# Kernel optimization log

Hardware: AMD Instinct MI355X
Metric: run time of the kernel (lower is better)

## Reference

```python
import jax, jax.numpy as jnp
import numpy as np

UP = 2
CUTOFF = 1.0 / UP  # factor = 1


def make_recon_rect(N, cutoff):
    """Reconstruction low-pass rect for rfft2, shape [N, N//2+1]."""
    lo = int(N * cutoff // 2)
    hi = int(N - lo)
    r = np.ones(N, dtype=np.float32)
    r[lo + 1:hi] = 0.0
    if N % 4 == 0:
        r[lo] = 0.5
        r[hi] = 0.5
    rect2d = r[:, None] * r[None, :]          # [N, N]
    return jnp.asarray(rect2d[:, :N // 2 + 1])  # keep rfft half-spectrum


def setup_inputs() -> dict:
    key = jax.random.key(0)
    x = jax.random.normal(key, (16, 64, 128, 128), dtype=jnp.float32)
    return {"x": x}


def reference(x):
    B, C, H, W = x.shape
    Hu, Wu = H * UP, W * UP
    # zero-insertion upsample: sample at (i*UP, j*UP), zeros elsewhere
    z = jnp.zeros((B, C, Hu, Wu), dtype=x.dtype).at[:, :, ::UP, ::UP].set(x)
    rect = make_recon_rect(Wu, CUTOFF)         # [Wu, Wu//2+1]
    xf = jnp.fft.rfft2(z) * rect               # low-pass in frequency domain
    out = jnp.fft.irfft2(xf) * (UP ** 2)       # gain correction
    return out
```

## Files before the change

### kernel.cpp

```cpp
#include <hip/hip_runtime.h>


typedef __bf16 bf16x8 __attribute__((ext_vector_type(8)));
typedef float  f32x4  __attribute__((ext_vector_type(4)));

#define W2 136
#define PI_F 3.14159265358979323846f

__device__ __forceinline__ unsigned short f2bf(float x) {
    unsigned int b = __float_as_uint(x);
    return (unsigned short)((b + 0x7FFFu + ((b >> 16) & 1u)) >> 16);
}

__device__ __forceinline__ float gfun(int j) {
    int d = 2 * (j & 127) + 1;
    float th = PI_F * (float)d * (1.0f / 256.0f);
    float s  = ((d & 3) == 1) ? 1.0f : -1.0f;
    return s * cosf(th) / (128.0f * sinf(th));
}

__global__ __launch_bounds__(512)
void init_ghtab(unsigned short* __restrict__ ghtab)
{
    const int t    = threadIdx.x;
    const int lane = t & 63;
    const int l15  = lane & 15;
    const int l4   = lane >> 4;
    const int dd   = t >> 6;
    const int base = l15 - 8 * l4 + 16 * dd;
    unsigned short u[8];
    #pragma unroll
    for (int e = 0; e < 8; ++e) u[e] = f2bf(gfun(base - e));
    *(ushort4*)&ghtab[t * 8]     = make_ushort4(u[0], u[1], u[2], u[3]);
    *(ushort4*)&ghtab[t * 8 + 4] = make_ushort4(u[4], u[5], u[6], u[7]);
}

__global__ __launch_bounds__(512, 4)
void upsample_fused(const float* __restrict__ xin, float* __restrict__ out,
                    const unsigned short* __restrict__ ghtab)
{
    __shared__ __align__(16) unsigned short Et[128 * W2];

    const int tid  = threadIdx.x;
    const int lane = tid & 63;
    const int w    = tid >> 6;
    const int l15  = lane & 15;
    const int l4   = lane >> 4;

    const long long img = blockIdx.x >> 1;
    const int cb        = blockIdx.x & 1;
    const float* __restrict__ xim = xin + img * (128LL * 128LL);
    float*       __restrict__ oim = out + img * (256LL * 256LL);

    const int r = 16 * w + l15;
    const float* __restrict__ xrow = xim + r * 128;

    float4 xlo[4], xhi[4];
    #pragma unroll
    for (int t = 0; t < 4; ++t) {
        xlo[t] = *(const float4*)&xrow[32 * t + 8 * l4];
        xhi[t] = *(const float4*)&xrow[32 * t + 8 * l4 + 4];
    }

    bf16x8 ghc[8];
    #pragma unroll
    for (int v = 0; v < 8; ++v) {
        const int dd = (v + 4 * cb) & 7;
        ghc[v] = *(const bf16x8*)&ghtab[(dd * 64 + lane) * 8];
    }

    bf16x8 xa[4];
    #pragma unroll
    for (int t = 0; t < 4; ++t) {
        union { bf16x8 v; unsigned short u[8]; } H;
        H.u[0] = f2bf(xlo[t].x); H.u[1] = f2bf(xlo[t].y);
        H.u[2] = f2bf(xlo[t].z); H.u[3] = f2bf(xlo[t].w);
        H.u[4] = f2bf(xhi[t].x); H.u[5] = f2bf(xhi[t].y);
        H.u[6] = f2bf(xhi[t].z); H.u[7] = f2bf(xhi[t].w);
        xa[t] = H.v;
        if ((t >> 1) == cb) {
            const int tt = t & 1;
            #pragma unroll
            for (int e = 0; e < 8; ++e)
                Et[(64 * tt + 16 * l4 + 2 * e) * W2 + r] = H.u[e];
        }
    }

    float* __restrict__ orow = oim + (2 * r) * 256 + 128 * cb;
    #pragma unroll
    for (int mt = 0; mt < 4; ++mt) {
        f32x4 acc = {0.f, 0.f, 0.f, 0.f};
        #pragma unroll
        for (int t = 0; t < 4; ++t)
            acc = __builtin_amdgcn_mfma_f32_16x16x32_bf16(ghc[(mt - 2 * t) & 7],
                                                          xa[t], acc, 0, 0, 0);
        const int i0l = 16 * mt + 4 * l4;
        float4 xc = *(const float4*)&xrow[64 * cb + i0l];
        float4 o0 = make_float4(xc.x, acc[0], xc.y, acc[1]);
        float4 o1 = make_float4(xc.z, acc[2], xc.w, acc[3]);
        *(float4*)&orow[2 * i0l]     = o0;
        *(float4*)&orow[2 * i0l + 4] = o1;
        #pragma unroll
        for (int q = 0; q < 4; ++q)
            Et[(2 * (i0l + q) + 1) * W2 + r] = f2bf(acc[q]);
    }
    __syncthreads();

    {
        bf16x8 gb[4];
        #pragma unroll
        for (int t = 0; t < 4; ++t) {
            const int dd = (w - 2 * t) & 7;
            gb[t] = *(const bf16x8*)&ghtab[(dd * 64 + lane) * 8];
        }
        float* __restrict__ prow = oim + (2 * (16 * w + l15) + 1) * 256 + 128 * cb;
        #pragma unroll
        for (int mc = 0; mc < 8; ++mc) {
            f32x4 acc = {0.f, 0.f, 0.f, 0.f};
            #pragma unroll
            for (int t = 0; t < 4; ++t) {
                bf16x8 ef = *(const bf16x8*)&Et[(16 * mc + l15) * W2 + 32 * t + 8 * l4];
                acc = __builtin_amdgcn_mfma_f32_16x16x32_bf16(ef, gb[t], acc, 0, 0, 0);
            }
            float4 o = make_float4(acc[0], acc[1], acc[2], acc[3]);
            *(float4*)&prow[16 * mc + 4 * l4] = o;
        }
    }
}

extern "C" void kernel_launch(void* const* d_in, const int* in_sizes, int n_in,
                              void* d_out, int out_size, void* d_ws, size_t ws_size,
                              hipStream_t stream)
{
    (void)n_in; (void)out_size; (void)ws_size;
    const float* x = (const float*)d_in[0];
    float* out = (float*)d_out;
    int nimg = in_sizes[0] / (128 * 128);

    unsigned short* ghtab = (unsigned short*)d_ws;
    hipLaunchKernelGGL(init_ghtab, dim3(1), dim3(512), 0, stream, ghtab);
    hipLaunchKernelGGL(upsample_fused, dim3(nimg * 2), dim3(512), 0, stream, x, out, ghtab);
}
```

Before: 96.92 us.

## Swizzle transposed LDS tile and reuse E fragments across two output row blocks

Replaces the padded LDS transpose buffer (stride 136) with an unpadded 128-wide layout using an XOR swizzle to avoid bank conflicts on the scattered column writes and vector row reads. The second-stage GEMM is reorganized so each wave handles two output row blocks and half the column tiles, so each LDS fragment load feeds two MFMAs. This halves LDS reads in phase two and cuts LDS size, at the cost of more XOR address arithmetic.

```diff
diff --git a/kernel.cpp b/kernel.cpp
--- a/kernel.cpp
+++ b/kernel.cpp
@@ -4,7 +4,6 @@
 typedef __bf16 bf16x8 __attribute__((ext_vector_type(8)));
 typedef float  f32x4  __attribute__((ext_vector_type(4)));
 
-#define W2 136
 #define PI_F 3.14159265358979323846f
 
 __device__ __forceinline__ unsigned short f2bf(float x) {
@@ -17,6 +16,10 @@
     float th = PI_F * (float)d * (1.0f / 256.0f);
     float s  = ((d & 3) == 1) ? 1.0f : -1.0f;
     return s * cosf(th) / (128.0f * sinf(th));
+}
+
+__device__ __forceinline__ int etswz(int row) {
+    return (((row & 7) ^ (((row >> 3) & 3) << 1) ^ (((row >> 5) & 1) << 2)) << 4);
 }
 
 __global__ __launch_bounds__(512)
@@ -39,7 +42,7 @@
 void upsample_fused(const float* __restrict__ xin, float* __restrict__ out,
                     const unsigned short* __restrict__ ghtab)
 {
-    __shared__ __align__(16) unsigned short Et[128 * W2];
+    __shared__ __align__(16) unsigned short Et[128 * 128];
 
     const int tid  = threadIdx.x;
     const int lane = tid & 63;
@@ -81,8 +84,10 @@
         if ((t >> 1) == cb) {
             const int tt = t & 1;
             #pragma unroll
-            for (int e = 0; e < 8; ++e)
-                Et[(64 * tt + 16 * l4 + 2 * e) * W2 + r] = H.u[e];
+            for (int e = 0; e < 8; ++e) {
+                const int row = 64 * tt + 16 * l4 + 2 * e;
+                Et[row * 128 + (((2 * r) ^ etswz(row)) >> 1)] = H.u[e];
+            }
         }
     }
 
@@ -101,29 +106,42 @@
         *(float4*)&orow[2 * i0l]     = o0;
         *(float4*)&orow[2 * i0l + 4] = o1;
         #pragma unroll
-        for (int q = 0; q < 4; ++q)
-            Et[(2 * (i0l + q) + 1) * W2 + r] = f2bf(acc[q]);
+        for (int q = 0; q < 4; ++q) {
+            const int row = 2 * (i0l + q) + 1;
+            Et[row * 128 + (((2 * r) ^ etswz(row)) >> 1)] = f2bf(acc[q]);
+        }
     }
     __syncthreads();
 
     {
-        bf16x8 gb[4];
+        const int pa = w & 3;
+        const int mh = w >> 2;
+        bf16x8 gbd[4];
         #pragma unroll
-        for (int t = 0; t < 4; ++t) {
-            const int dd = (w - 2 * t) & 7;
-            gb[t] = *(const bf16x8*)&ghtab[(dd * 64 + lane) * 8];
+        for (int d = 0; d < 4; ++d) {
+            const int dd = (pa + 2 * d) & 7;
+            gbd[d] = *(const bf16x8*)&ghtab[(dd * 64 + lane) * 8];
         }
-        float* __restrict__ prow = oim + (2 * (16 * w + l15) + 1) * 256 + 128 * cb;
+        float* __restrict__ prowA = oim + (2 * (16 * pa + l15) + 1) * 256 + 128 * cb;
+        float* __restrict__ prowB = oim + (2 * (16 * (pa + 4) + l15) + 1) * 256 + 128 * cb;
         #pragma unroll
-        for (int mc = 0; mc < 8; ++mc) {
-            f32x4 acc = {0.f, 0.f, 0.f, 0.f};
+        for (int mci = 0; mci < 4; ++mci) {
+            const int mc = 4 * mh + mci;
+            const int row = 16 * mc + l15;
+            const char* erow = (const char*)Et + row * 256;
+            const int sw = etswz(row);
+            f32x4 aA = {0.f, 0.f, 0.f, 0.f};
+            f32x4 aB = {0.f, 0.f, 0.f, 0.f};
             #pragma unroll
             for (int t = 0; t < 4; ++t) {
-                bf16x8 ef = *(const bf16x8*)&Et[(16 * mc + l15) * W2 + 32 * t + 8 * l4];
-                acc = __builtin_amdgcn_mfma_f32_16x16x32_bf16(ef, gb[t], acc, 0, 0, 0);
+                bf16x8 ef = *(const bf16x8*)(erow + (((64 * t + 16 * l4)) ^ sw));
+                aA = __builtin_amdgcn_mfma_f32_16x16x32_bf16(ef, gbd[(-t) & 3], aA, 0, 0, 0);
+                aB = __builtin_amdgcn_mfma_f32_16x16x32_bf16(ef, gbd[(2 - t) & 3], aB, 0, 0, 0);
             }
-            float4 o = make_float4(acc[0], acc[1], acc[2], acc[3]);
-            *(float4*)&prow[16 * mc + 4 * l4] = o;
+            float4 oA = make_float4(aA[0], aA[1], aA[2], aA[3]);
+            float4 oB = make_float4(aB[0], aB[1], aB[2], aB[3]);
+            *(float4*)&prowA[16 * mc + 4 * l4] = oA;
+            *(float4*)&prowB[16 * mc + 4 * l4] = oB;
         }
     }
 }
```

Measured after the change: 95.36 us. No clear change (-1.6%).
